# Performance work log

Measured on AMD Instinct MI355X. Metric: run time of the kernel, lower is better.

Reference implementation:

```python
import jax, jax.numpy as jnp
import numpy as np

D_MODEL = 1024
NUM_HEADS = 16
HEAD_DIM = D_MODEL // NUM_HEADS


def setup_inputs() -> dict:
    key = jax.random.key(0)
    ks = jax.random.split(key, 5)
    x = jax.random.normal(ks[0], (2, 2048, D_MODEL), dtype=jnp.float32)
    # torch nn.Linear init scale ~ U(-1/sqrt(in), 1/sqrt(in)); use small normals
    s = 1.0 / np.sqrt(D_MODEL)
    W_qkv = jax.random.normal(ks[1], (D_MODEL, 3 * D_MODEL), dtype=jnp.float32) * s
    b_qkv = jax.random.normal(ks[2], (3 * D_MODEL,), dtype=jnp.float32) * s
    W_out = jax.random.normal(ks[3], (D_MODEL, D_MODEL), dtype=jnp.float32) * s
    b_out = jax.random.normal(ks[4], (D_MODEL,), dtype=jnp.float32) * s
    return {"x": x, "W_qkv": W_qkv, "b_qkv": b_qkv, "W_out": W_out, "b_out": b_out}


def reference(x, W_qkv, b_qkv, W_out, b_out):
    B, S, _ = x.shape
    qkv = x @ W_qkv + b_qkv                                  # [B,S,3D]
    qkv = qkv.reshape(B, S, NUM_HEADS, 3 * HEAD_DIM).transpose(0, 2, 1, 3)  # [B,H,S,3d]
    q, k, v = jnp.split(qkv, 3, axis=-1)                     # each [B,H,S,d]
    scale = 1.0 / np.sqrt(HEAD_DIM)
    scores = jnp.einsum("bhqd,bhkd->bhqk", q, k) * scale      # [B,H,S,S]
    attn = jax.nn.softmax(scores, axis=-1)
    values = jnp.einsum("bhqk,bhkd->bhqd", attn, v)           # [B,H,S,d]
    values = values.transpose(0, 2, 1, 3).reshape(B, S, D_MODEL)
    return values @ W_out + b_out
```

## Files before the change

### kernel.cpp

```cpp
#include <hip/hip_runtime.h>


#define D_MODEL 1024
#define NHEAD   16
#define HDIM    64
#define SEQ     2048
#define BATCH   2
#define NTOK    (BATCH * SEQ)

typedef float    f32x4  __attribute__((ext_vector_type(4)));
typedef float    f32x16 __attribute__((ext_vector_type(16)));
typedef _Float16 f16x8  __attribute__((ext_vector_type(8)));
typedef _Float16 f16x4  __attribute__((ext_vector_type(4)));

#define GLOBAL_LOAD_LDS16(gptr, lptr)                                            \
    __builtin_amdgcn_global_load_lds(                                            \
        (const __attribute__((address_space(1))) unsigned int*)(gptr),           \
        (__attribute__((address_space(3))) unsigned int*)(lptr), 16, 0, 0)

__global__ __launch_bounds__(256) void prep_kernel(
    const float* __restrict__ x, _Float16* __restrict__ xh,
    const float* __restrict__ Wqkv, _Float16* __restrict__ wq_t,
    const float* __restrict__ Wout, _Float16* __restrict__ wo_t)
{
    const int bx = blockIdx.x;
    const int tid = threadIdx.x;
    if (bx < 4096) {
        const int i = (bx * 256 + tid) * 4;
        const float4 v = *(const float4*)&x[i];
        f16x4 hh;
        hh[0] = (_Float16)v.x; hh[1] = (_Float16)v.y;
        hh[2] = (_Float16)v.z; hh[3] = (_Float16)v.w;
        *(f16x4*)&xh[i] = hh;
        return;
    }
    __shared__ float ts[64][65];
    const float* W; _Float16* Wt; int N, n0, k0;
    if (bx < 4096 + 768) {
        const int local = bx - 4096;
        W = Wqkv; Wt = wq_t; N = 3072;
        n0 = (local % 48) * 64; k0 = (local / 48) * 64;
    } else {
        const int local = bx - 4864;
        W = Wout; Wt = wo_t; N = 1024;
        n0 = (local % 16) * 64; k0 = (local / 16) * 64;
    }
    {
        const int r = tid >> 2, c = (tid & 3) << 4;
        const float* src = W + (size_t)(k0 + r) * N + n0 + c;
        #pragma unroll
        for (int u = 0; u < 4; ++u)
            *(float4*)&ts[r][c + u * 4] = *(const float4*)&src[u * 4];
    }
    __syncthreads();
    {
        const int n = tid >> 2, kg = (tid & 3) << 4;
        f16x8 v0, v1;
        #pragma unroll
        for (int j = 0; j < 8; ++j) {
            v0[j] = (_Float16)ts[kg + j][n];
            v1[j] = (_Float16)ts[kg + 8 + j][n];
        }
        _Float16* dst = Wt + (size_t)(n0 + n) * D_MODEL + k0 + kg;
        *(f16x8*)&dst[0] = v0;
        *(f16x8*)&dst[8] = v1;
    }
}

__global__ __launch_bounds__(512) void gemm_qkv_kernel(
    const _Float16* __restrict__ A, const _Float16* __restrict__ Bt,
    const float* __restrict__ bias, _Float16* __restrict__ Cout,
    int M, int N, int K)
{
    __shared__ _Float16 lds[3][2][4096];
    const int tid = threadIdx.x;
    const int wave = tid >> 6, lane = tid & 63;
    const int quad = lane >> 4, l16 = lane & 15;
    const int m0 = blockIdx.y * 128, n0 = blockIdx.x * 128;
    const int wr = wave >> 1, wc = wave & 1;

    f32x4 acc[2][4] = {};

    const bool isA = wave < 4;
    const _Float16* gsrc = isA ? (A + (size_t)m0 * K) : (Bt + (size_t)n0 * K);
    const int plane = isA ? 0 : 1;
    const int sbase = (wave & 3) * 2;

#define G1_STAGE(tt, bi) {                                                     \
        const int _k1 = (tt) * 32;                                             \
        _Pragma("unroll")                                                      \
        for (int _j = 0; _j < 2; ++_j) {                                       \
            const int _seg = sbase + _j;                                       \
            const int _row = ((_seg & 1) << 6) | lane;                         \
            GLOBAL_LOAD_LDS16(gsrc + (size_t)_row * K + _k1 + (_seg >> 1) * 8, \
                              &lds[bi][plane][_seg * 512]);                    \
        } }

#define G1_COMPUTE(bi) {                                                       \
        f16x8 a[2], b[4];                                                      \
        _Pragma("unroll")                                                      \
        for (int mt = 0; mt < 2; ++mt)                                         \
            a[mt] = *(const f16x8*)&lds[bi][0][quad * 1024 + (wr * 32 + mt * 16 + l16) * 8]; \
        _Pragma("unroll")                                                      \
        for (int nt = 0; nt < 4; ++nt)                                         \
            b[nt] = *(const f16x8*)&lds[bi][1][quad * 1024 + (wc * 64 + nt * 16 + l16) * 8]; \
        __builtin_amdgcn_s_setprio(1);                                         \
        _Pragma("unroll")                                                      \
        for (int mt = 0; mt < 2; ++mt)                                         \
            _Pragma("unroll")                                                  \
            for (int nt = 0; nt < 4; ++nt)                                     \
                acc[mt][nt] = __builtin_amdgcn_mfma_f32_16x16x32_f16(a[mt], b[nt], acc[mt][nt], 0, 0, 0); \
        __builtin_amdgcn_s_setprio(0); }

#define G1_KSTEP(t, gatestr) {                                                 \
        const int _cur = (t) % 3;                                              \
        if ((t) + 2 < nk) { G1_STAGE((t) + 2, ((t) + 2) % 3); }                \
        asm volatile("s_waitcnt " gatestr ::: "memory");                       \
        __builtin_amdgcn_s_barrier();                                          \
        __builtin_amdgcn_sched_barrier(0);                                     \
        G1_COMPUTE(_cur);                                                      \
        __builtin_amdgcn_sched_barrier(0);                                     \
        __builtin_amdgcn_s_barrier();                                          \
        __builtin_amdgcn_sched_barrier(0);                                     \
    }

    const int nk = K / 32;
    G1_STAGE(0, 0);
    G1_STAGE(1, 1);

    for (int t = 0; t < nk - 2; ++t)
        G1_KSTEP(t, "vmcnt(4)");
    G1_KSTEP(nk - 2, "vmcnt(2)");
    G1_KSTEP(nk - 1, "vmcnt(0)");

#undef G1_KSTEP
#undef G1_COMPUTE
#undef G1_STAGE

    #pragma unroll
    for (int nt = 0; nt < 4; ++nt) {
        const int col = n0 + wc * 64 + nt * 16 + l16;
        const float bv = bias[col];
        #pragma unroll
        for (int mt = 0; mt < 2; ++mt) {
            #pragma unroll
            for (int r = 0; r < 4; ++r) {
                const int row = m0 + wr * 32 + mt * 16 + quad * 4 + r;
                Cout[(size_t)row * N + col] = (_Float16)(acc[mt][nt][r] + bv);
            }
        }
    }
}

__global__ __launch_bounds__(512) void gemm_out_kernel(
    const _Float16* __restrict__ A, const _Float16* __restrict__ Bt,
    const float* __restrict__ bias, float* __restrict__ Cout)
{
    const int K = D_MODEL, N = D_MODEL;
    __shared__ _Float16 ldsA[2][4096];
    __shared__ _Float16 ldsB[2][2048];
    const int tid = threadIdx.x;
    const int wave = tid >> 6, lane = tid & 63;
    const int quad = lane >> 4, l16 = lane & 15;
    const int m0 = blockIdx.y * 128, n0 = blockIdx.x * 64;
    const int wr = wave >> 1, wc = wave & 1;

    f32x4 acc[2][2] = {};

    if (wave < 4) {
        #pragma unroll
        for (int j = 0; j < 2; ++j) {
            const int seg = wave * 2 + j;
            const int chunk = seg >> 1;
            const int row = ((seg & 1) << 6) | lane;
            GLOBAL_LOAD_LDS16(A + (size_t)(m0 + row) * K + chunk * 8, &ldsA[0][seg * 512]);
        }
    } else {
        const int seg = wave - 4;
        GLOBAL_LOAD_LDS16(Bt + (size_t)(n0 + lane) * K + seg * 8, &ldsB[0][seg * 512]);
    }
    __syncthreads();

    const int nk = K / 32;
    for (int t = 0; t < nk; ++t) {
        const int cur = t & 1;

        if (t + 1 < nk) {
            const int k1 = (t + 1) * 32;
            if (wave < 4) {
                #pragma unroll
                for (int j = 0; j < 2; ++j) {
                    const int seg = wave * 2 + j;
                    const int chunk = seg >> 1;
                    const int row = ((seg & 1) << 6) | lane;
                    GLOBAL_LOAD_LDS16(A + (size_t)(m0 + row) * K + k1 + chunk * 8,
                                      &ldsA[cur ^ 1][seg * 512]);
                }
            } else {
                const int seg = wave - 4;
                GLOBAL_LOAD_LDS16(Bt + (size_t)(n0 + lane) * K + k1 + seg * 8,
                                  &ldsB[cur ^ 1][seg * 512]);
            }
        }

        f16x8 a[2], b[2];
        #pragma unroll
        for (int mt = 0; mt < 2; ++mt)
            a[mt] = *(const f16x8*)&ldsA[cur][quad * 1024 + (wr * 32 + mt * 16 + l16) * 8];
        #pragma unroll
        for (int nt = 0; nt < 2; ++nt)
            b[nt] = *(const f16x8*)&ldsB[cur][quad * 512 + (wc * 32 + nt * 16 + l16) * 8];
        #pragma unroll
        for (int mt = 0; mt < 2; ++mt)
            #pragma unroll
            for (int nt = 0; nt < 2; ++nt)
                acc[mt][nt] = __builtin_amdgcn_mfma_f32_16x16x32_f16(a[mt], b[nt], acc[mt][nt], 0, 0, 0);

        __syncthreads();
    }

    #pragma unroll
    for (int nt = 0; nt < 2; ++nt) {
        const int col = n0 + wc * 32 + nt * 16 + l16;
        const float bv = bias[col];
        #pragma unroll
        for (int mt = 0; mt < 2; ++mt) {
            #pragma unroll
            for (int r = 0; r < 4; ++r) {
                const int row = m0 + wr * 32 + mt * 16 + quad * 4 + r;
                Cout[(size_t)row * N + col] = acc[mt][nt][r] + bv;
            }
        }
    }
}

__global__ __launch_bounds__(256) void swizzle_kv_kernel(
    const _Float16* __restrict__ qkv,
    _Float16* __restrict__ Ksw, _Float16* __restrict__ Vsw)
{
    __shared__ _Float16 ts[64][72];
    const int tid = threadIdx.x;
    const int s0 = blockIdx.x * 64, h = blockIdx.y, b = blockIdx.z;
    const size_t hsz = (size_t)8 * SEQ * 8;
    _Float16* kh = Ksw + (size_t)(b * NHEAD + h) * hsz;
    _Float16* vh = Vsw + (size_t)(b * NHEAD + h) * hsz;

    {
        const int s = s0 + (tid >> 2);
        const int dg = (tid & 3) << 4;
        const _Float16* src = qkv + (size_t)(b * SEQ + s) * (3 * D_MODEL) + h * (3 * HDIM) + HDIM + dg;
        const f16x8 v0 = *(const f16x8*)&src[0];
        const f16x8 v1 = *(const f16x8*)&src[8];
        const int c0 = dg >> 3;
        *(f16x8*)&kh[((size_t)c0 * SEQ + s) * 8]       = v0;
        *(f16x8*)&kh[((size_t)(c0 + 1) * SEQ + s) * 8] = v1;
    }
    {
        const int s = tid >> 2, dg = (tid & 3) << 4;
        const _Float16* src = qkv + (size_t)(b * SEQ + s0 + s) * (3 * D_MODEL) + h * (3 * HDIM) + 2 * HDIM + dg;
        *(f16x8*)&ts[s][dg]     = *(const f16x8*)&src[0];
        *(f16x8*)&ts[s][dg + 8] = *(const f16x8*)&src[8];
    }
    __syncthreads();
    {
        const int d = tid >> 2, sg = (tid & 3) << 4;
        f16x8 v0, v1;
        #pragma unroll
        for (int j = 0; j < 8; ++j) { v0[j] = ts[sg + j][d]; v1[j] = ts[sg + 8 + j][d]; }
        const int cs0 = (s0 + sg) >> 3;
        *(f16x8*)&vh[((size_t)cs0 * HDIM + d) * 8]       = v0;
        *(f16x8*)&vh[((size_t)(cs0 + 1) * HDIM + d) * 8] = v1;
    }
}

__device__ __forceinline__ void softmax_frag(
    const f32x16 s0, const f32x16 s1, float& rs, f16x8 pa[4])
{
    #pragma unroll
    for (int half = 0; half < 2; ++half) {
        const f32x16 sv = half ? s1 : s0;
        float p[16];
        #pragma unroll
        for (int r = 0; r < 16; ++r)
            p[r] = __builtin_amdgcn_exp2f(sv[r]);
        #pragma unroll
        for (int r = 0; r < 16; r += 4)
            rs += (p[r] + p[r + 1]) + (p[r + 2] + p[r + 3]);

        union { f16x8 hv; unsigned u[4]; } lo, hh;
        {
            const unsigned A = __builtin_bit_cast(unsigned, __builtin_amdgcn_cvt_pkrtz(p[0], p[1]));
            const unsigned B = __builtin_bit_cast(unsigned, __builtin_amdgcn_cvt_pkrtz(p[2], p[3]));
            const unsigned C = __builtin_bit_cast(unsigned, __builtin_amdgcn_cvt_pkrtz(p[4], p[5]));
            const unsigned D = __builtin_bit_cast(unsigned, __builtin_amdgcn_cvt_pkrtz(p[6], p[7]));
            const auto rac = __builtin_amdgcn_permlane32_swap(A, C, false, false);
            const auto rbd = __builtin_amdgcn_permlane32_swap(B, D, false, false);
            lo.u[0] = rac[0]; lo.u[1] = rbd[0]; lo.u[2] = rac[1]; lo.u[3] = rbd[1];
        }
        {
            const unsigned E = __builtin_bit_cast(unsigned, __builtin_amdgcn_cvt_pkrtz(p[8],  p[9]));
            const unsigned F = __builtin_bit_cast(unsigned, __builtin_amdgcn_cvt_pkrtz(p[10], p[11]));
            const unsigned G = __builtin_bit_cast(unsigned, __builtin_amdgcn_cvt_pkrtz(p[12], p[13]));
            const unsigned H = __builtin_bit_cast(unsigned, __builtin_amdgcn_cvt_pkrtz(p[14], p[15]));
            const auto reg = __builtin_amdgcn_permlane32_swap(E, G, false, false);
            const auto rfh = __builtin_amdgcn_permlane32_swap(F, H, false, false);
            hh.u[0] = reg[0]; hh.u[1] = rfh[0]; hh.u[2] = reg[1]; hh.u[3] = rfh[1];
        }
        pa[half * 2]     = lo.hv;
        pa[half * 2 + 1] = hh.hv;
    }
}

__global__ __launch_bounds__(512) void attn_mfma_kernel(
    const _Float16* __restrict__ qkv,
    const _Float16* __restrict__ Ksw, const _Float16* __restrict__ Vsw,
    _Float16* __restrict__ val)
{
    __shared__ _Float16 Ks[2][8192];
    __shared__ _Float16 Vts[2][8192];

    const int tid = threadIdx.x;
    const int wave = tid >> 6, lane = tid & 63;
    const int l31 = lane & 31, hi = lane >> 5;

    const int id = blockIdx.x;
    const int g  = (id & 7) * 32 + (id >> 3);
    const int qt = g & 7, hb = g >> 3;
    const int h  = hb & 15, b = hb >> 4;
    const int q0 = qt * 256;

    const size_t hsz = (size_t)8 * SEQ * 8;
    const _Float16* kh = Ksw + (size_t)(b * NHEAD + h) * hsz;
    const _Float16* vh = Vsw + (size_t)(b * NHEAD + h) * hsz;

    f16x8 qf[4];
    {
        const int row = q0 + wave * 32 + l31;
        const _Float16* src = qkv + (size_t)(b * SEQ + row) * (3 * D_MODEL) + h * (3 * HDIM) + hi * 8;
        #pragma unroll
        for (int kk = 0; kk < 4; ++kk) {
            const f16x8 t = *(const f16x8*)(src + kk * 16);
            #pragma unroll
            for (int j = 0; j < 8; ++j)
                qf[kk][j] = (_Float16)((float)t[j] * 0.1803368802f);
        }
    }

    f32x16 acc0 = {};
    f32x16 acc1 = {};
    float rs = 0.f;

    const int sidx0 = wave * 2;
    #pragma unroll
    for (int j = 0; j < 2; ++j) {
        const int idx = sidx0 + j;
        const int u = idx >> 3, c = idx & 7;
        GLOBAL_LOAD_LDS16(kh + ((size_t)c * SEQ + u * 64 + lane) * 8, &Ks[0][idx * 512]);
        GLOBAL_LOAD_LDS16(vh + ((size_t)(u * 8 + c) * HDIM + lane) * 8, &Vts[0][idx * 512]);
    }
    __syncthreads();

    for (int kt = 0; kt < SEQ / 128; ++kt) {
        const int cur = kt & 1;

        if (kt + 1 < SEQ / 128) {
            #pragma unroll
            for (int j = 0; j < 2; ++j) {
                const int idx = sidx0 + j;
                const int u = idx >> 3, c = idx & 7;
                GLOBAL_LOAD_LDS16(kh + ((size_t)c * SEQ + (kt + 1) * 128 + u * 64 + lane) * 8,
                                  &Ks[cur ^ 1][idx * 512]);
                GLOBAL_LOAD_LDS16(vh + ((size_t)((kt + 1) * 16 + u * 8 + c) * HDIM + lane) * 8,
                                  &Vts[cur ^ 1][idx * 512]);
            }
        }

        #pragma unroll
        for (int u = 0; u < 2; ++u) {
            const _Float16* ksub = &Ks[cur][u * 4096];
            const _Float16* vsub = &Vts[cur][u * 4096];

            f32x16 s0 = {}, s1 = {};
            __builtin_amdgcn_s_setprio(1);
            #pragma unroll
            for (int kk = 0; kk < 4; ++kk) {
                const f16x8 k0 = *(const f16x8*)&ksub[(kk * 2 + hi) * 512 + l31 * 8];
                const f16x8 k1 = *(const f16x8*)&ksub[(kk * 2 + hi) * 512 + (32 + l31) * 8];
                s0 = __builtin_amdgcn_mfma_f32_32x32x16_f16(k0, qf[kk], s0, 0, 0, 0);
                s1 = __builtin_amdgcn_mfma_f32_32x32x16_f16(k1, qf[kk], s1, 0, 0, 0);
            }
            __builtin_amdgcn_s_setprio(0);

            f16x8 pa[4];
            softmax_frag(s0, s1, rs, pa);

            __builtin_amdgcn_s_setprio(1);
            #pragma unroll
            for (int ks = 0; ks < 4; ++ks) {
                const f16x8 v0 = *(const f16x8*)&vsub[(ks * 2 + hi) * 512 + l31 * 8];
                const f16x8 v1 = *(const f16x8*)&vsub[(ks * 2 + hi) * 512 + (32 + l31) * 8];
                acc0 = __builtin_amdgcn_mfma_f32_32x32x16_f16(pa[ks], v0, acc0, 0, 0, 0);
                acc1 = __builtin_amdgcn_mfma_f32_32x32x16_f16(pa[ks], v1, acc1, 0, 0, 0);
            }
            __builtin_amdgcn_s_setprio(0);
        }

        __syncthreads();
    }

    rs += __shfl_xor(rs, 32);
    const float inv = 1.f / rs;

    #pragma unroll
    for (int r = 0; r < 16; ++r) {
        const int qo = (r & 3) + 8 * (r >> 2) + 4 * hi;
        const float invr = __shfl(inv, qo);
        const int row = b * SEQ + q0 + wave * 32 + qo;
        val[(size_t)row * D_MODEL + h * HDIM + l31]      = (_Float16)(acc0[r] * invr);
        val[(size_t)row * D_MODEL + h * HDIM + 32 + l31] = (_Float16)(acc1[r] * invr);
    }
}

extern "C" void kernel_launch(void* const* d_in, const int* in_sizes, int n_in,
                              void* d_out, int out_size, void* d_ws, size_t ws_size,
                              hipStream_t stream)
{
    const float* x     = (const float*)d_in[0];
    const float* W_qkv = (const float*)d_in[1];
    const float* b_qkv = (const float*)d_in[2];
    const float* W_out = (const float*)d_in[3];
    const float* b_out = (const float*)d_in[4];

    char* ws = (char*)d_ws;
    _Float16* Ksw   = (_Float16*)ws;
    _Float16* val_h = (_Float16*)(ws + (8u << 20));
    _Float16* wq_t  = (_Float16*)(ws + (16u << 20));
    _Float16* wo_t  = (_Float16*)(ws + (22u << 20));
    _Float16* qkv_h = (_Float16*)(ws + (24u << 20));
    _Float16* x_h   = (_Float16*)(ws + (48u << 20));
    _Float16* Vsw   = (_Float16*)(ws + (48u << 20));

    prep_kernel<<<5120, 256, 0, stream>>>(x, x_h, W_qkv, wq_t, W_out, wo_t);
    gemm_qkv_kernel<<<dim3(3 * D_MODEL / 128, NTOK / 128), 512, 0, stream>>>(
        x_h, wq_t, b_qkv, qkv_h, NTOK, 3 * D_MODEL, D_MODEL);
    swizzle_kv_kernel<<<dim3(SEQ / 64, NHEAD, BATCH), 256, 0, stream>>>(qkv_h, Ksw, Vsw);
    attn_mfma_kernel<<<dim3(256, 1, 1), 512, 0, stream>>>(qkv_h, Ksw, Vsw, val_h);
    gemm_out_kernel<<<dim3(D_MODEL / 64, NTOK / 128), 512, 0, stream>>>(
        val_h, wo_t, b_out, (float*)d_out);
}
```

Measured before the change: 211.5 us.

## Fuse K/V swizzle into QKV GEMM epilogue and drop swizzle kernel

The QKV GEMM epilogue now writes Q to a compact per-head buffer and scatters K and V straight into the swizzled layouts the attention kernel reads. This removes the separate swizzle kernel launch and the round trip through a full qkv intermediate in global memory. The cost is scattered, poorly coalesced 2-byte stores for K (stride 8 halves), and the workspace layout is reshuffled.

```diff
diff --git a/kernel.cpp b/kernel.cpp
--- a/kernel.cpp
+++ b/kernel.cpp
@@ -69,7 +69,8 @@
 
 __global__ __launch_bounds__(512) void gemm_qkv_kernel(
     const _Float16* __restrict__ A, const _Float16* __restrict__ Bt,
-    const float* __restrict__ bias, _Float16* __restrict__ Cout,
+    const float* __restrict__ bias, _Float16* __restrict__ Qh,
+    _Float16* __restrict__ Ksw, _Float16* __restrict__ Vsw,
     int M, int N, int K)
 {
     __shared__ _Float16 lds[3][2][4096];
@@ -137,16 +138,57 @@
 #undef G1_COMPUTE
 #undef G1_STAGE
 
-    #pragma unroll
-    for (int nt = 0; nt < 4; ++nt) {
-        const int col = n0 + wc * 64 + nt * 16 + l16;
-        const float bv = bias[col];
-        #pragma unroll
-        for (int mt = 0; mt < 2; ++mt) {
-            #pragma unroll
-            for (int r = 0; r < 4; ++r) {
-                const int row = m0 + wr * 32 + mt * 16 + quad * 4 + r;
-                Cout[(size_t)row * N + col] = (_Float16)(acc[mt][nt][r] + bv);
+    const int colb = n0 + wc * 64;
+    const int kind = (colb >> 6) % 3;
+    const int h    = colb / 192;
+    const int bb   = m0 >> 11;
+    const int m0r  = m0 & 2047;
+    const size_t hsz = (size_t)8 * SEQ * 8;
+
+    if (kind == 0) {
+        _Float16* qh = Qh + (size_t)m0 * D_MODEL + h * HDIM;
+        #pragma unroll
+        for (int nt = 0; nt < 4; ++nt) {
+            const float bv = bias[colb + nt * 16 + l16];
+            #pragma unroll
+            for (int mt = 0; mt < 2; ++mt) {
+                #pragma unroll
+                for (int r = 0; r < 4; ++r) {
+                    const int row = wr * 32 + mt * 16 + quad * 4 + r;
+                    qh[(size_t)row * D_MODEL + nt * 16 + l16] = (_Float16)(acc[mt][nt][r] + bv);
+                }
+            }
+        }
+    } else if (kind == 1) {
+        _Float16* kh = Ksw + (size_t)(bb * NHEAD + h) * hsz;
+        #pragma unroll
+        for (int nt = 0; nt < 4; ++nt) {
+            const int d = nt * 16 + l16;
+            const float bv = bias[colb + nt * 16 + l16];
+            _Float16* kd = kh + (size_t)(d >> 3) * (SEQ * 8) + (d & 7);
+            #pragma unroll
+            for (int mt = 0; mt < 2; ++mt) {
+                #pragma unroll
+                for (int r = 0; r < 4; ++r) {
+                    const int s = m0r + wr * 32 + mt * 16 + quad * 4 + r;
+                    kd[(size_t)s * 8] = (_Float16)(acc[mt][nt][r] + bv);
+                }
+            }
+        }
+    } else {
+        _Float16* vh = Vsw + (size_t)(bb * NHEAD + h) * hsz;
+        #pragma unroll
+        for (int nt = 0; nt < 4; ++nt) {
+            const int d = nt * 16 + l16;
+            const float bv = bias[colb + nt * 16 + l16];
+            #pragma unroll
+            for (int mt = 0; mt < 2; ++mt) {
+                const int s0 = m0r + wr * 32 + mt * 16 + quad * 4;
+                f16x4 pk;
+                #pragma unroll
+                for (int r = 0; r < 4; ++r)
+                    pk[r] = (_Float16)(acc[mt][nt][r] + bv);
+                *(f16x4*)&vh[(size_t)(s0 >> 3) * 512 + d * 8 + (s0 & 7)] = pk;
             }
         }
     }
@@ -234,45 +276,6 @@
     }
 }
 
-__global__ __launch_bounds__(256) void swizzle_kv_kernel(
-    const _Float16* __restrict__ qkv,
-    _Float16* __restrict__ Ksw, _Float16* __restrict__ Vsw)
-{
-    __shared__ _Float16 ts[64][72];
-    const int tid = threadIdx.x;
-    const int s0 = blockIdx.x * 64, h = blockIdx.y, b = blockIdx.z;
-    const size_t hsz = (size_t)8 * SEQ * 8;
-    _Float16* kh = Ksw + (size_t)(b * NHEAD + h) * hsz;
-    _Float16* vh = Vsw + (size_t)(b * NHEAD + h) * hsz;
-
-    {
-        const int s = s0 + (tid >> 2);
-        const int dg = (tid & 3) << 4;
-        const _Float16* src = qkv + (size_t)(b * SEQ + s) * (3 * D_MODEL) + h * (3 * HDIM) + HDIM + dg;
-        const f16x8 v0 = *(const f16x8*)&src[0];
-        const f16x8 v1 = *(const f16x8*)&src[8];
-        const int c0 = dg >> 3;
-        *(f16x8*)&kh[((size_t)c0 * SEQ + s) * 8]       = v0;
-        *(f16x8*)&kh[((size_t)(c0 + 1) * SEQ + s) * 8] = v1;
-    }
-    {
-        const int s = tid >> 2, dg = (tid & 3) << 4;
-        const _Float16* src = qkv + (size_t)(b * SEQ + s0 + s) * (3 * D_MODEL) + h * (3 * HDIM) + 2 * HDIM + dg;
-        *(f16x8*)&ts[s][dg]     = *(const f16x8*)&src[0];
-        *(f16x8*)&ts[s][dg + 8] = *(const f16x8*)&src[8];
-    }
-    __syncthreads();
-    {
-        const int d = tid >> 2, sg = (tid & 3) << 4;
-        f16x8 v0, v1;
-        #pragma unroll
-        for (int j = 0; j < 8; ++j) { v0[j] = ts[sg + j][d]; v1[j] = ts[sg + 8 + j][d]; }
-        const int cs0 = (s0 + sg) >> 3;
-        *(f16x8*)&vh[((size_t)cs0 * HDIM + d) * 8]       = v0;
-        *(f16x8*)&vh[((size_t)(cs0 + 1) * HDIM + d) * 8] = v1;
-    }
-}
-
 __device__ __forceinline__ void softmax_frag(
     const f32x16 s0, const f32x16 s1, float& rs, f16x8 pa[4])
 {
@@ -312,7 +315,7 @@
 }
 
 __global__ __launch_bounds__(512) void attn_mfma_kernel(
-    const _Float16* __restrict__ qkv,
+    const _Float16* __restrict__ Qh,
     const _Float16* __restrict__ Ksw, const _Float16* __restrict__ Vsw,
     _Float16* __restrict__ val)
 {
@@ -336,7 +339,7 @@
     f16x8 qf[4];
     {
         const int row = q0 + wave * 32 + l31;
-        const _Float16* src = qkv + (size_t)(b * SEQ + row) * (3 * D_MODEL) + h * (3 * HDIM) + hi * 8;
+        const _Float16* src = Qh + (size_t)(b * SEQ + row) * D_MODEL + h * HDIM + hi * 8;
         #pragma unroll
         for (int kk = 0; kk < 4; ++kk) {
             const f16x8 t = *(const f16x8*)(src + kk * 16);
@@ -436,15 +439,14 @@
     _Float16* val_h = (_Float16*)(ws + (8u << 20));
     _Float16* wq_t  = (_Float16*)(ws + (16u << 20));
     _Float16* wo_t  = (_Float16*)(ws + (22u << 20));
-    _Float16* qkv_h = (_Float16*)(ws + (24u << 20));
-    _Float16* x_h   = (_Float16*)(ws + (48u << 20));
-    _Float16* Vsw   = (_Float16*)(ws + (48u << 20));
+    _Float16* q_h   = (_Float16*)(ws + (24u << 20));
+    _Float16* x_h   = (_Float16*)(ws + (32u << 20));
+    _Float16* Vsw   = (_Float16*)(ws + (40u << 20));
 
     prep_kernel<<<5120, 256, 0, stream>>>(x, x_h, W_qkv, wq_t, W_out, wo_t);
     gemm_qkv_kernel<<<dim3(3 * D_MODEL / 128, NTOK / 128), 512, 0, stream>>>(
-        x_h, wq_t, b_qkv, qkv_h, NTOK, 3 * D_MODEL, D_MODEL);
-    swizzle_kv_kernel<<<dim3(SEQ / 64, NHEAD, BATCH), 256, 0, stream>>>(qkv_h, Ksw, Vsw);
-    attn_mfma_kernel<<<dim3(256, 1, 1), 512, 0, stream>>>(qkv_h, Ksw, Vsw, val_h);
+        x_h, wq_t, b_qkv, q_h, Ksw, Vsw, NTOK, 3 * D_MODEL, D_MODEL);
+    attn_mfma_kernel<<<dim3(256, 1, 1), 512, 0, stream>>>(q_h, Ksw, Vsw, val_h);
     gemm_out_kernel<<<dim3(D_MODEL / 64, NTOK / 128), 512, 0, stream>>>(
         val_h, wo_t, b_out, (float*)d_out);
 }
```

New measurement: 202.8 us. -4.1%, faster.
